# Optimization experiments

Hardware: AMD Instinct MI355X
Metric: run time of the kernel (lower is better)

## Reference

```python
import jax, jax.numpy as jnp
import numpy as np

B, L, C, H = 8, 1024, 384, 6
D = C // H          # head_dim = 64
K, N = 2, 4         # radial_degree, angular_degree
EPS = 1e-5


def setup_inputs() -> dict:
    key = jax.random.key(0)
    ks = jax.random.split(key, 8)
    x = jax.random.normal(ks[0], (B, L, C), dtype=jnp.float32)
    pos = jax.random.uniform(ks[1], (B, L, 2), dtype=jnp.float32) * 32.0
    w_norm = jnp.ones((C,), dtype=jnp.float32)
    w_in = jax.random.normal(ks[2], (3 * C, C), dtype=jnp.float32) * 0.02
    b_in = jnp.zeros((3 * C,), dtype=jnp.float32)
    w_out = jax.random.normal(ks[3], (C, C), dtype=jnp.float32) * 0.02
    b_out = jnp.zeros((C,), dtype=jnp.float32)
    b_coef = jax.random.normal(ks[4], (H, K + 1, N + 1), dtype=jnp.float32) * 0.01
    b_coef = b_coef.at[:, 1, 0].set(1.0)  # reset_parameters fills b[..., 1, 0] = 1
    c_coef = jax.random.normal(ks[5], (H, K + 1, N + 1), dtype=jnp.float32) * 0.01
    return {"x": x, "pos": pos, "w_norm": w_norm, "w_in": w_in, "b_in": b_in,
            "w_out": w_out, "b_out": b_out, "b_coef": b_coef, "c_coef": c_coef}


def _polar_bias(pos, b_coef, c_coef):
    # pos: (B, L, 2) -> bias grid (B, H, L, L)
    dist = pos[:, :, None, :] - pos[:, None, :, :]           # (B, Lq, Lk, 2)
    theta = jnp.arctan2(dist[..., 1], dist[..., 0])          # (B, Lq, Lk)
    r = jnp.sqrt(jnp.sum(dist * dist, axis=-1))              # (B, Lq, Lk)
    r_pow = r[..., None] ** jnp.arange(K + 1, dtype=r.dtype)           # (B, Lq, Lk, K+1)
    ang = theta[..., None] * jnp.arange(N + 1, dtype=theta.dtype)      # (B, Lq, Lk, N+1)
    cos_part = jnp.einsum('hkn,bijk,bijn->bhij', b_coef, r_pow, jnp.cos(ang))
    sin_part = jnp.einsum('hkn,bijk,bijn->bhij', c_coef, r_pow, jnp.sin(ang))
    return cos_part + sin_part


def reference(x, pos, w_norm, w_in, b_in, w_out, b_out, b_coef, c_coef):
    # RMSNorm
    ms = jnp.mean(x * x, axis=-1, keepdims=True)
    xn = x * jax.lax.rsqrt(ms + EPS) * w_norm
    # packed QKV projection
    qkv = xn @ w_in.T + b_in                                  # (B, L, 3C)
    q, k, v = jnp.split(qkv, 3, axis=-1)
    def heads(t):  # (B, L, C) -> (B, H, L, D)
        return t.reshape(B, L, H, D).transpose(0, 2, 1, 3)
    q, k, v = heads(q), heads(k), heads(v)
    bias = _polar_bias(pos, b_coef, c_coef)                   # (B, H, L, L)
    scores = jnp.einsum('bhqd,bhkd->bhqk', q, k) / jnp.sqrt(jnp.float32(D)) + bias
    attn = jax.nn.softmax(scores, axis=-1)
    o = jnp.einsum('bhqk,bhkd->bhqd', attn, v)                # (B, H, L, D)
    o = o.transpose(0, 2, 1, 3).reshape(B, L, C)
    return o @ w_out.T + b_out
```

## Files before the change

kernel.cpp:

```cpp
#include <hip/hip_runtime.h>

typedef unsigned int  u32;
typedef unsigned short u16;
typedef __attribute__((ext_vector_type(8))) short short8;
typedef __attribute__((ext_vector_type(4))) float f32x4;

__device__ __forceinline__ u16 f2bf(float x) {
  union { float f; u32 u; } un; un.f = x;
  u32 r = un.u + 0x7FFFu + ((un.u >> 16) & 1u);
  return (u16)(r >> 16);
}
__device__ __forceinline__ u32 cvtpk(float lo, float hi) {
  u32 r;
  asm("v_cvt_pk_bf16_f32 %0, %1, %2" : "=v"(r) : "v"(lo), "v"(hi));
  return r;
}
__device__ __forceinline__ f32x4 mfma_bf16(short8 a, short8 b, f32x4 c) {
  return __builtin_amdgcn_mfma_f32_16x16x32_bf16(a, b, c, 0, 0, 0);
}

__global__ __launch_bounds__(256) void prep_kernel(
    const float* __restrict__ x, const float* __restrict__ w_norm,
    const float* __restrict__ w_in, const float* __restrict__ w_out,
    u16* __restrict__ xn, u16* __restrict__ winb, u16* __restrict__ woutb)
{
  int blk = blockIdx.x, t = threadIdx.x;
  if (blk < 2048) {
    int wv = t >> 6, lane = t & 63;
    int row = blk * 4 + wv;
    const float* xr = x + (size_t)row * 384;
    float v[6]; float ss = 0.f;
    #pragma unroll
    for (int i = 0; i < 6; i++) { v[i] = xr[lane + 64 * i]; ss += v[i] * v[i]; }
    #pragma unroll
    for (int off = 32; off > 0; off >>= 1) ss += __shfl_xor(ss, off);
    float rs = __builtin_amdgcn_rsqf(ss * (1.0f / 384.0f) + 1e-5f);
    #pragma unroll
    for (int i = 0; i < 6; i++) {
      float xv = v[i] * rs * w_norm[lane + 64 * i];
      xn[(size_t)row * 384 + lane + 64 * i] = f2bf(xv);
    }
  } else {
    int base = (blk - 2048) * 2048 + t * 8;
    #pragma unroll
    for (int j = 0; j < 8; j++) {
      int idx = base + j;
      if (idx < 442368) winb[idx] = f2bf(w_in[idx]);
      else              woutb[idx - 442368] = f2bf(w_out[idx - 442368]);
    }
  }
}

template<bool OUT_F32, bool QSCALE>
__global__ __launch_bounds__(256) void gemm_kernel(
    const u16* __restrict__ A, int lda,
    const u16* __restrict__ Bw, int ldb,
    const float* __restrict__ bias, void* __restrict__ outp, int ldc, int K)
{
  __shared__ __attribute__((aligned(16))) u16 As[128 * 72];
  __shared__ __attribute__((aligned(16))) u16 Bs[128 * 72];
  int t = threadIdx.x;
  int lane = t & 63, wv = t >> 6;
  int g = lane >> 4, cl = lane & 15;
  int row0 = blockIdx.x * 128, col0 = blockIdx.y * 128;
  int wm = (wv >> 1) * 64, wn = (wv & 1) * 64;
  f32x4 acc[4][4];
  #pragma unroll
  for (int i = 0; i < 4; i++)
    #pragma unroll
    for (int j = 0; j < 4; j++) acc[i][j] = (f32x4){0.f, 0.f, 0.f, 0.f};

  for (int k0 = 0; k0 < K; k0 += 64) {
    __syncthreads();
    #pragma unroll
    for (int j = 0; j < 4; j++) {
      int i = t + 256 * j;
      int r = i >> 3, ch = i & 7;
      *(uint4*)(&As[r * 72 + ch * 8]) =
          *(const uint4*)(A + (size_t)(row0 + r) * lda + k0 + ch * 8);
      *(uint4*)(&Bs[r * 72 + ch * 8]) =
          *(const uint4*)(Bw + (size_t)(col0 + r) * ldb + k0 + ch * 8);
    }
    __syncthreads();
    #pragma unroll
    for (int kh = 0; kh < 2; kh++) {
      short8 af[4], bfr[4];
      #pragma unroll
      for (int s = 0; s < 4; s++) {
        af[s]  = *(const short8*)(&As[(wm + s * 16 + cl) * 72 + kh * 32 + g * 8]);
        bfr[s] = *(const short8*)(&Bs[(wn + s * 16 + cl) * 72 + kh * 32 + g * 8]);
      }
      #pragma unroll
      for (int i = 0; i < 4; i++)
        #pragma unroll
        for (int j = 0; j < 4; j++)
          acc[i][j] = mfma_bf16(af[i], bfr[j], acc[i][j]);
    }
  }
  #pragma unroll
  for (int i = 0; i < 4; i++) {
    #pragma unroll
    for (int j = 0; j < 4; j++) {
      int colb = col0 + wn + j * 16 + cl;
      float bv = bias[colb];
      #pragma unroll
      for (int r = 0; r < 4; r++) {
        int rowb = row0 + wm + i * 16 + g * 4 + r;
        float v = acc[i][j][r] + bv;
        if (QSCALE) { if (colb < 384) v *= 0.125f; }
        if (OUT_F32) ((float*)outp)[(size_t)rowb * ldc + colb] = v;
        else ((u16*)outp)[(size_t)rowb * ldc + colb] = f2bf(v);
      }
    }
  }
}

__global__ __launch_bounds__(256) void attn_swap3(
    const u16* __restrict__ qkv, const float* __restrict__ pos,
    const float* __restrict__ bcf, const float* __restrict__ ccf,
    u16* __restrict__ obuf)
{
  __shared__ __attribute__((aligned(16))) u16 vsmem[4][64][40];
  __shared__ float mlbuf[2][2][16];

  int bid = blockIdx.x;
  int xslot = bid & 7, rest = bid >> 3;
  int qt = rest & 31, gdiv = rest >> 5;
  int g48 = gdiv * 8 + xslot;
  int b = g48 / 6, h = g48 - b * 6;

  int t = threadIdx.x, lane = t & 63, wv = t >> 6;
  int strip = wv & 1, half = wv >> 1;
  int g = lane >> 4, cl = lane & 15;

  float bc[15], cc[15];
  #pragma unroll
  for (int i = 0; i < 15; i++) { bc[i] = bcf[h * 15 + i]; cc[i] = ccf[h * 15 + i]; }

  int qrow = qt * 32 + strip * 16 + cl;
  const u16* qbase = qkv + (size_t)(b * 1024 + qrow) * 1152 + h * 64;
  short8 qf0 = *(const short8*)(qbase + g * 8);
  short8 qf1 = *(const short8*)(qbase + 32 + g * 8);
  float qx = pos[(size_t)(b * 1024 + qrow) * 2 + 0];
  float qy = pos[(size_t)(b * 1024 + qrow) * 2 + 1];

  f32x4 oa[4];
  #pragma unroll
  for (int d = 0; d < 4; d++) oa[d] = (f32x4){0.f, 0.f, 0.f, 0.f};
  float m_own = -1e30f, l_own = 0.f;

  const u16* kb = qkv + (size_t)b * 1024 * 1152 + 384 + h * 64;
  int kappa = lane & 31, dh = lane >> 5;
  const u16* vsrc = qkv + (size_t)b * 1024 * 1152 + 768 + h * 64 + dh * 32;
  const float* pb = pos + (size_t)b * 2048;

  int pcol = (kappa & 3) | ((kappa & 0x0C) << 1) | ((kappa & 0x10) >> 2);
  u16* vdst = &vsmem[wv][dh * 32][0] + pcol;

  for (int it = 0; it < 16; it++) {
    int k0 = half * 512 + it * 32;
    {
      const u16* vr = vsrc + (size_t)(k0 + kappa) * 1152;
      uint4 a0 = *(const uint4*)(vr);
      uint4 a1 = *(const uint4*)(vr + 8);
      uint4 a2 = *(const uint4*)(vr + 16);
      uint4 a3 = *(const uint4*)(vr + 24);
      #define ST(i, val) vdst[(i) * 40] = (u16)(val)
      ST(0,  a0.x); ST(1,  a0.x >> 16); ST(2,  a0.y); ST(3,  a0.y >> 16);
      ST(4,  a0.z); ST(5,  a0.z >> 16); ST(6,  a0.w); ST(7,  a0.w >> 16);
      ST(8,  a1.x); ST(9,  a1.x >> 16); ST(10, a1.y); ST(11, a1.y >> 16);
      ST(12, a1.z); ST(13, a1.z >> 16); ST(14, a1.w); ST(15, a1.w >> 16);
      ST(16, a2.x); ST(17, a2.x >> 16); ST(18, a2.y); ST(19, a2.y >> 16);
      ST(20, a2.z); ST(21, a2.z >> 16); ST(22, a2.w); ST(23, a2.w >> 16);
      ST(24, a3.x); ST(25, a3.x >> 16); ST(26, a3.y); ST(27, a3.y >> 16);
      ST(28, a3.z); ST(29, a3.z >> 16); ST(30, a3.w); ST(31, a3.w >> 16);
      #undef ST
    }
    f32x4 sk[2];
    #pragma unroll
    for (int ks = 0; ks < 2; ks++) {
      const u16* kr = kb + (size_t)(k0 + ks * 16 + cl) * 1152;
      short8 kf0 = *(const short8*)(kr + g * 8);
      short8 kf1 = *(const short8*)(kr + 32 + g * 8);
      f32x4 z = (f32x4){0.f, 0.f, 0.f, 0.f};
      z = mfma_bf16(kf0, qf0, z);
      z = mfma_bf16(kf1, qf1, z);
      sk[ks] = z;
    }
    #pragma unroll
    for (int ks = 0; ks < 2; ks++) {
      int kb4 = k0 + ks * 16 + 4 * g;
      float4 pA = *(const float4*)(pb + (size_t)kb4 * 2);
      float4 pB = *(const float4*)(pb + (size_t)kb4 * 2 + 4);
      float kxs[4] = {pA.x, pA.z, pB.x, pB.z};
      float kys[4] = {pA.y, pA.w, pB.y, pB.w};
      #pragma unroll
      for (int r = 0; r < 4; r++) {
        float dx = qx - kxs[r], dy = qy - kys[r];
        float r2 = dx * dx + dy * dy;
        bool zz = !(r2 > 0.f);
        float ir = zz ? 0.f : __builtin_amdgcn_rsqf(r2);
        float rr = r2 * ir;
        float c1 = zz ? 1.f : dx * ir;
        float s1 = dy * ir;
        float tc = c1 + c1;
        float c2 = __builtin_fmaf(tc, c1, -1.f), s2 = tc * s1;
        float c3 = __builtin_fmaf(tc, c2, -c1),  s3 = __builtin_fmaf(tc, s2, -s1);
        float c4 = __builtin_fmaf(tc, c3, -c2),  s4 = __builtin_fmaf(tc, s3, -s2);
        float a0 = bc[0] + bc[1]*c1 + bc[2]*c2 + bc[3]*c3 + bc[4]*c4
                 + cc[1]*s1 + cc[2]*s2 + cc[3]*s3 + cc[4]*s4;
        float a1 = bc[5] + bc[6]*c1 + bc[7]*c2 + bc[8]*c3 + bc[9]*c4
                 + cc[6]*s1 + cc[7]*s2 + cc[8]*s3 + cc[9]*s4;
        float a2 = bc[10] + bc[11]*c1 + bc[12]*c2 + bc[13]*c3 + bc[14]*c4
                 + cc[11]*s1 + cc[12]*s2 + cc[13]*s3 + cc[14]*s4;
        sk[ks][r] += a0 + rr * __builtin_fmaf(rr, a2, a1);
      }
    }
    float tmax = -1e30f;
    #pragma unroll
    for (int ks = 0; ks < 2; ks++)
      #pragma unroll
      for (int r = 0; r < 4; r++) tmax = fmaxf(tmax, sk[ks][r]);
    if (!__all((int)(tmax <= m_own + 8.f))) {
      tmax = fmaxf(tmax, __shfl_xor(tmax, 16));
      tmax = fmaxf(tmax, __shfl_xor(tmax, 32));
      float mn = fmaxf(m_own, tmax);
      float sc = __builtin_amdgcn_exp2f((m_own - mn) * 1.44269504f);
      m_own = mn;
      l_own *= sc;
      #pragma unroll
      for (int r = 0; r < 4; r++) {
        float scr = __shfl(sc, 4 * g + r);
        #pragma unroll
        for (int d = 0; d < 4; d++) oa[d][r] *= scr;
      }
    }
    float psum = 0.f;
    #pragma unroll
    for (int ks = 0; ks < 2; ks++)
      #pragma unroll
      for (int r = 0; r < 4; r++) {
        float p = __builtin_amdgcn_exp2f((sk[ks][r] - m_own) * 1.44269504f);
        psum += p; sk[ks][r] = p;
      }
    l_own += psum;
    union { u32 w[4]; short8 s8; } pk;
    pk.w[0] = cvtpk(sk[0][0], sk[0][1]); pk.w[1] = cvtpk(sk[0][2], sk[0][3]);
    pk.w[2] = cvtpk(sk[1][0], sk[1][1]); pk.w[3] = cvtpk(sk[1][2], sk[1][3]);
    #pragma unroll
    for (int d = 0; d < 4; d++) {
      short8 vf = *(const short8*)(&vsmem[wv][d * 16 + cl][g * 8]);
      oa[d] = mfma_bf16(pk.s8, vf, oa[d]);
    }
  }
  l_own += __shfl_xor(l_own, 16);
  l_own += __shfl_xor(l_own, 32);
  __syncthreads();
  float* o1 = (float*)&vsmem[0][0][0];
  if (half == 1) {
    if (lane < 16) { mlbuf[0][strip][lane] = m_own; mlbuf[1][strip][lane] = l_own; }
    #pragma unroll
    for (int r = 0; r < 4; r++) {
      int row = 4 * g + r;
      #pragma unroll
      for (int d = 0; d < 4; d++)
        o1[(strip * 16 + row) * 64 + d * 16 + cl] = oa[d][r];
    }
  }
  __syncthreads();
  if (half == 0) {
    float m1 = mlbuf[0][strip][cl], l1 = mlbuf[1][strip][cl];
    float M  = fmaxf(m_own, m1);
    float f0 = __builtin_amdgcn_exp2f((m_own - M) * 1.44269504f);
    float f1 = __builtin_amdgcn_exp2f((m1    - M) * 1.44269504f);
    float linv = __builtin_amdgcn_rcpf(l_own * f0 + l1 * f1);
    #pragma unroll
    for (int r = 0; r < 4; r++) {
      int row = 4 * g + r;
      float f0r = __shfl(f0, row), f1r = __shfl(f1, row), invr = __shfl(linv, row);
      int qr = qt * 32 + strip * 16 + row;
      #pragma unroll
      for (int d = 0; d < 4; d++) {
        float val = (oa[d][r] * f0r +
                     o1[(strip * 16 + row) * 64 + d * 16 + cl] * f1r) * invr;
        obuf[(size_t)(b * 1024 + qr) * 384 + h * 64 + d * 16 + cl] = f2bf(val);
      }
    }
  }
}

extern "C" void kernel_launch(void* const* d_in, const int* in_sizes, int n_in,
                              void* d_out, int out_size, void* d_ws, size_t ws_size,
                              hipStream_t stream) {
  const float* x      = (const float*)d_in[0];
  const float* pos    = (const float*)d_in[1];
  const float* w_norm = (const float*)d_in[2];
  const float* w_in   = (const float*)d_in[3];
  const float* b_in   = (const float*)d_in[4];
  const float* w_out  = (const float*)d_in[5];
  const float* b_out  = (const float*)d_in[6];
  const float* b_coef = (const float*)d_in[7];
  const float* c_coef = (const float*)d_in[8];

  char* ws = (char*)d_ws;
  u16* xn    = (u16*)(ws + 0);
  u16* obuf  = (u16*)(ws + 0);
  u16* winb  = (u16*)(ws + 6291456);
  u16* woutb = (u16*)(ws + 7176192);
  u16* qkvb  = (u16*)(ws + 7471104);

  prep_kernel<<<2336, 256, 0, stream>>>(x, w_norm, w_in, w_out, xn, winb, woutb);
  gemm_kernel<false, true><<<dim3(64, 9), 256, 0, stream>>>(
      xn, 384, winb, 384, b_in, qkvb, 1152, 384);
  attn_swap3<<<1536, 256, 0, stream>>>(qkvb, pos, b_coef, c_coef, obuf);
  gemm_kernel<true, false><<<dim3(64, 3), 256, 0, stream>>>(
      obuf, 384, woutb, 384, b_out, (float*)d_out, 384, 384);
}
```

Before: 155.5 us.

## Split attention key range four ways per 16-row query tile

The attention kernel now gives each block a single 16-row query tile, with each of its four waves covering a quarter of the keys (256 each). Previously a block held two 16-row strips and split the keys in halves. The grid doubles to 3072 blocks, and the per-wave partial softmax states are combined by wave 0 through shared memory. Loop addressing also moves to incremental 32-bit offsets. This shortens each wave's serial key loop and adds parallelism, at the cost of a heavier four-way merge step and repeated K/V/pos loads across twice as many blocks.

```diff
diff --git a/kernel.cpp b/kernel.cpp
--- a/kernel.cpp
+++ b/kernel.cpp
@@ -115,29 +115,27 @@
   }
 }
 
-__global__ __launch_bounds__(256) void attn_swap3(
+__global__ __launch_bounds__(256) void attn_swap4(
     const u16* __restrict__ qkv, const float* __restrict__ pos,
     const float* __restrict__ bcf, const float* __restrict__ ccf,
     u16* __restrict__ obuf)
 {
   __shared__ __attribute__((aligned(16))) u16 vsmem[4][64][40];
-  __shared__ float mlbuf[2][2][16];
 
   int bid = blockIdx.x;
   int xslot = bid & 7, rest = bid >> 3;
-  int qt = rest & 31, gdiv = rest >> 5;
+  int qt16 = rest & 63, gdiv = rest >> 6;
   int g48 = gdiv * 8 + xslot;
   int b = g48 / 6, h = g48 - b * 6;
 
   int t = threadIdx.x, lane = t & 63, wv = t >> 6;
-  int strip = wv & 1, half = wv >> 1;
   int g = lane >> 4, cl = lane & 15;
 
   float bc[15], cc[15];
   #pragma unroll
   for (int i = 0; i < 15; i++) { bc[i] = bcf[h * 15 + i]; cc[i] = ccf[h * 15 + i]; }
 
-  int qrow = qt * 32 + strip * 16 + cl;
+  int qrow = qt16 * 16 + cl;
   const u16* qbase = qkv + (size_t)(b * 1024 + qrow) * 1152 + h * 64;
   short8 qf0 = *(const short8*)(qbase + g * 8);
   short8 qf1 = *(const short8*)(qbase + 32 + g * 8);
@@ -151,16 +149,19 @@
 
   const u16* kb = qkv + (size_t)b * 1024 * 1152 + 384 + h * 64;
   int kappa = lane & 31, dh = lane >> 5;
-  const u16* vsrc = qkv + (size_t)b * 1024 * 1152 + 768 + h * 64 + dh * 32;
+  const u16* vb = qkv + (size_t)b * 1024 * 1152 + 768 + h * 64 + dh * 32;
   const float* pb = pos + (size_t)b * 2048;
 
   int pcol = (kappa & 3) | ((kappa & 0x0C) << 1) | ((kappa & 0x10) >> 2);
   u16* vdst = &vsmem[wv][dh * 32][0] + pcol;
 
-  for (int it = 0; it < 16; it++) {
-    int k0 = half * 512 + it * 32;
+  u32 koff = (u32)(wv * 256 + cl) * 1152;
+  u32 voff = (u32)(wv * 256 + kappa) * 1152;
+  u32 poff = (u32)(wv * 256 + 4 * g) * 2;
+
+  for (int it = 0; it < 8; it++) {
     {
-      const u16* vr = vsrc + (size_t)(k0 + kappa) * 1152;
+      const u16* vr = vb + voff;
       uint4 a0 = *(const uint4*)(vr);
       uint4 a1 = *(const uint4*)(vr + 8);
       uint4 a2 = *(const uint4*)(vr + 16);
@@ -179,7 +180,7 @@
     f32x4 sk[2];
     #pragma unroll
     for (int ks = 0; ks < 2; ks++) {
-      const u16* kr = kb + (size_t)(k0 + ks * 16 + cl) * 1152;
+      const u16* kr = kb + koff + ks * (16 * 1152);
       short8 kf0 = *(const short8*)(kr + g * 8);
       short8 kf1 = *(const short8*)(kr + 32 + g * 8);
       f32x4 z = (f32x4){0.f, 0.f, 0.f, 0.f};
@@ -189,9 +190,8 @@
     }
     #pragma unroll
     for (int ks = 0; ks < 2; ks++) {
-      int kb4 = k0 + ks * 16 + 4 * g;
-      float4 pA = *(const float4*)(pb + (size_t)kb4 * 2);
-      float4 pB = *(const float4*)(pb + (size_t)kb4 * 2 + 4);
+      float4 pA = *(const float4*)(pb + poff + ks * 32);
+      float4 pB = *(const float4*)(pb + poff + ks * 32 + 4);
       float kxs[4] = {pA.x, pA.z, pB.x, pB.z};
       float kys[4] = {pA.y, pA.w, pB.y, pB.w};
       #pragma unroll
@@ -216,6 +216,7 @@
         sk[ks][r] += a0 + rr * __builtin_fmaf(rr, a2, a1);
       }
     }
+    koff += 32 * 1152; voff += 32 * 1152; poff += 64;
     float tmax = -1e30f;
     #pragma unroll
     for (int ks = 0; ks < 2; ks++)
@@ -257,32 +258,40 @@
   l_own += __shfl_xor(l_own, 32);
   __syncthreads();
   float* o1 = (float*)&vsmem[0][0][0];
-  if (half == 1) {
-    if (lane < 16) { mlbuf[0][strip][lane] = m_own; mlbuf[1][strip][lane] = l_own; }
+  float* ml = (float*)((char*)&vsmem[0][0][0] + 19968);
+  if (lane < 16) { ml[wv * 16 + lane] = m_own; ml[64 + wv * 16 + lane] = l_own; }
+  if (wv > 0) {
     #pragma unroll
     for (int r = 0; r < 4; r++) {
       int row = 4 * g + r;
       #pragma unroll
       for (int d = 0; d < 4; d++)
-        o1[(strip * 16 + row) * 64 + d * 16 + cl] = oa[d][r];
+        o1[((wv - 1) * 16 + row) * 64 + d * 16 + cl] = oa[d][r];
     }
   }
   __syncthreads();
-  if (half == 0) {
-    float m1 = mlbuf[0][strip][cl], l1 = mlbuf[1][strip][cl];
-    float M  = fmaxf(m_own, m1);
+  if (wv == 0) {
+    float m1 = ml[16 + cl], m2 = ml[32 + cl], m3 = ml[48 + cl];
+    float l1 = ml[80 + cl], l2 = ml[96 + cl], l3 = ml[112 + cl];
+    float M  = fmaxf(fmaxf(m_own, m1), fmaxf(m2, m3));
     float f0 = __builtin_amdgcn_exp2f((m_own - M) * 1.44269504f);
-    float f1 = __builtin_amdgcn_exp2f((m1    - M) * 1.44269504f);
-    float linv = __builtin_amdgcn_rcpf(l_own * f0 + l1 * f1);
+    float f1 = __builtin_amdgcn_exp2f((m1 - M) * 1.44269504f);
+    float f2 = __builtin_amdgcn_exp2f((m2 - M) * 1.44269504f);
+    float f3 = __builtin_amdgcn_exp2f((m3 - M) * 1.44269504f);
+    float linv = __builtin_amdgcn_rcpf(l_own * f0 + l1 * f1 + l2 * f2 + l3 * f3);
     #pragma unroll
     for (int r = 0; r < 4; r++) {
       int row = 4 * g + r;
-      float f0r = __shfl(f0, row), f1r = __shfl(f1, row), invr = __shfl(linv, row);
-      int qr = qt * 32 + strip * 16 + row;
+      float f0r = __shfl(f0, row), f1r = __shfl(f1, row);
+      float f2r = __shfl(f2, row), f3r = __shfl(f3, row);
+      float invr = __shfl(linv, row);
+      int qr = qt16 * 16 + row;
       #pragma unroll
       for (int d = 0; d < 4; d++) {
-        float val = (oa[d][r] * f0r +
-                     o1[(strip * 16 + row) * 64 + d * 16 + cl] * f1r) * invr;
+        float val = (oa[d][r] * f0r
+                   + o1[(0 * 16 + row) * 64 + d * 16 + cl] * f1r
+                   + o1[(1 * 16 + row) * 64 + d * 16 + cl] * f2r
+                   + o1[(2 * 16 + row) * 64 + d * 16 + cl] * f3r) * invr;
         obuf[(size_t)(b * 1024 + qr) * 384 + h * 64 + d * 16 + cl] = f2bf(val);
       }
     }
@@ -312,7 +321,7 @@
   prep_kernel<<<2336, 256, 0, stream>>>(x, w_norm, w_in, w_out, xn, winb, woutb);
   gemm_kernel<false, true><<<dim3(64, 9), 256, 0, stream>>>(
       xn, 384, winb, 384, b_in, qkvb, 1152, 384);
-  attn_swap3<<<1536, 256, 0, stream>>>(qkvb, pos, b_coef, c_coef, obuf);
+  attn_swap4<<<3072, 256, 0, stream>>>(qkvb, pos, b_coef, c_coef, obuf);
   gemm_kernel<true, false><<<dim3(64, 3), 256, 0, stream>>>(
       obuf, 384, woutb, 384, b_out, (float*)d_out, 384, 384);
 }
```

After: 156.4 us (median of 2 runs). No clear change (+0.6%).
